# Kernel optimization log

Hardware: AMD Instinct MI355X
Metric: run time of the kernel (lower is better)

The kernel has to match this reference:

```python
import jax, jax.numpy as jnp
import numpy as np

N, E, F_IN, HID, HEADS, NT, B = 50000, 400000, 32, 64, 4, 20, 64
IN1 = F_IN + HID  # 96, conv1 input dim after concat with node-type embedding


def _glorot(key, shape):
    fan_in = shape[0]
    return jax.random.normal(key, shape, dtype=jnp.float32) / np.sqrt(fan_in)


def setup_inputs() -> dict:
    key = jax.random.key(0)
    ks = jax.random.split(key, 40)
    inp = {
        "x": jax.random.normal(ks[0], (N, F_IN), dtype=jnp.float32),
        "edge_index": jax.random.randint(ks[1], (2, E), 0, N, dtype=jnp.int32),
        "edge_attr": jax.random.normal(ks[2], (E,), dtype=jnp.float32),
        "batch": jnp.sort(jax.random.randint(ks[3], (N,), 0, B, dtype=jnp.int32)),
        "node_type": jax.random.randint(ks[4], (N,), 0, NT, dtype=jnp.int32),
        # parameters
        "node_emb": jax.random.normal(ks[5], (NT, HID), dtype=jnp.float32) * 0.1,
        "edge_W": _glorot(ks[6], (1, HID)), "edge_b": jnp.zeros((HID,), jnp.float32),
        # GATConv 1 (in=96, out=64, heads=4, edge_dim=64, concat=False)
        "W1": _glorot(ks[7], (IN1, HEADS * HID)),
        "att_src1": jax.random.normal(ks[8], (HEADS, HID), jnp.float32) * 0.1,
        "att_dst1": jax.random.normal(ks[9], (HEADS, HID), jnp.float32) * 0.1,
        "We1": _glorot(ks[10], (HID, HEADS * HID)),
        "att_e1": jax.random.normal(ks[11], (HEADS, HID), jnp.float32) * 0.1,
        "b1": jnp.zeros((HID,), jnp.float32),
        # GATConv 2 (in=64)
        "W2": _glorot(ks[12], (HID, HEADS * HID)),
        "att_src2": jax.random.normal(ks[13], (HEADS, HID), jnp.float32) * 0.1,
        "att_dst2": jax.random.normal(ks[14], (HEADS, HID), jnp.float32) * 0.1,
        "We2": _glorot(ks[15], (HID, HEADS * HID)),
        "att_e2": jax.random.normal(ks[16], (HEADS, HID), jnp.float32) * 0.1,
        "b2": jnp.zeros((HID,), jnp.float32),
        # SAGEConv (mean aggr): out = mean_agg @ Wl + x @ Wr + b
        "sage_Wl": _glorot(ks[17], (HID, HID)), "sage_Wr": _glorot(ks[18], (HID, HID)),
        "sage_b": jnp.zeros((HID,), jnp.float32),
        "lin1_W": _glorot(ks[19], (HID, HID)), "lin1_b": jnp.zeros((HID,), jnp.float32),
        "lin2_W": _glorot(ks[20], (HID, HID)), "lin2_b": jnp.zeros((HID,), jnp.float32),
        "tel_W": _glorot(ks[21], (HID, 1)), "tel_b": jnp.zeros((1,), jnp.float32),
        "comp_W": _glorot(ks[22], (HID, 1)), "comp_b": jnp.zeros((1,), jnp.float32),
        "pch_W": _glorot(ks[23], (HID, 1)), "pch_b": jnp.zeros((1,), jnp.float32),
    }
    return inp


def _gat(x, src, dst, edge_h, W, att_s, att_d, We, att_e, b):
    n = x.shape[0]
    h = (x @ W).reshape(n, HEADS, HID)                       # [N,H,C]
    a_s = (h * att_s).sum(-1)                                # [N,H]
    a_d = (h * att_d).sum(-1)
    e = (edge_h @ We).reshape(-1, HEADS, HID)                # [E,H,C]
    a_e = (e * att_e).sum(-1)                                # [E,H]
    alpha = jax.nn.leaky_relu(a_s[src] + a_d[dst] + a_e, 0.2)
    m = jax.ops.segment_max(alpha, dst, num_segments=n)
    m = jnp.where(jnp.isfinite(m), m, 0.0)
    ex = jnp.exp(alpha - m[dst])
    den = jax.ops.segment_sum(ex, dst, num_segments=n)
    alpha = ex / (den[dst] + 1e-16)                          # segment softmax per dst
    out = jax.ops.segment_sum(h[src] * alpha[..., None], dst, num_segments=n)
    return out.mean(axis=1) + b                              # concat=False -> head mean


def reference(x, edge_index, edge_attr, batch, node_type, node_emb, edge_W, edge_b,
              W1, att_src1, att_dst1, We1, att_e1, b1,
              W2, att_src2, att_dst2, We2, att_e2, b2,
              sage_Wl, sage_Wr, sage_b, lin1_W, lin1_b, lin2_W, lin2_b,
              tel_W, tel_b, comp_W, comp_b, pch_W, pch_b):
    src, dst = edge_index[0], edge_index[1]
    edge_h = edge_attr[:, None] @ edge_W + edge_b            # [E,HID]
    h = jnp.concatenate([x, node_emb[node_type]], axis=-1)   # [N,96]
    h = jax.nn.elu(_gat(h, src, dst, edge_h, W1, att_src1, att_dst1, We1, att_e1, b1))
    h = jax.nn.elu(_gat(h, src, dst, edge_h, W2, att_src2, att_dst2, We2, att_e2, b2))
    # SAGEConv with mean aggregation
    deg = jax.ops.segment_sum(jnp.ones((src.shape[0],), h.dtype), dst, num_segments=N)
    agg = jax.ops.segment_sum(h[src], dst, num_segments=N) / jnp.maximum(deg, 1.0)[:, None]
    h = jax.nn.elu(agg @ sage_Wl + h @ sage_Wr + sage_b)
    # global mean pool over graphs
    cnt = jax.ops.segment_sum(jnp.ones((N,), h.dtype), batch, num_segments=B)
    g = jax.ops.segment_sum(h, batch, num_segments=B) / jnp.maximum(cnt, 1.0)[:, None]
    g = jax.nn.elu(g @ lin1_W + lin1_b)                      # dropout is identity in eval
    g = g @ lin2_W + lin2_b
    return (g @ tel_W + tel_b, g @ comp_W + comp_b, g @ pch_W + pch_b)
```

## Files before the change

kernel.cpp:

```cpp
#include <hip/hip_runtime.h>
#include <hip/hip_bf16.h>


#define NN 50000
#define NE 400000
#define FIN 32
#define NBATCH 64

typedef __hip_bfloat16 bf16;
typedef short bf16x8 __attribute__((ext_vector_type(8)));
typedef float f32x4 __attribute__((ext_vector_type(4)));

__device__ __forceinline__ float b2f(bf16 v) { return __bfloat162float(v); }
__device__ __forceinline__ float lrelu(float x) { return x > 0.f ? x : 0.2f * x; }
__device__ __forceinline__ float eluf(float x) { return x > 0.f ? x : (expf(x) - 1.f); }

__device__ __forceinline__ float4 f4fma(float s, float4 w, float4 c) {
  c.x = fmaf(s, w.x, c.x); c.y = fmaf(s, w.y, c.y);
  c.z = fmaf(s, w.z, c.z); c.w = fmaf(s, w.w, c.w);
  return c;
}

__device__ __forceinline__ float4 upk4(uint2 u) {
  float4 f;
  f.x = __uint_as_float(u.x << 16);
  f.y = __uint_as_float(u.x & 0xffff0000u);
  f.z = __uint_as_float(u.y << 16);
  f.w = __uint_as_float(u.y & 0xffff0000u);
  return f;
}

__device__ __forceinline__ unsigned short bfbits(float f) {
  bf16 b = __float2bfloat16(f);
  unsigned short u;
  __builtin_memcpy(&u, &b, 2);
  return u;
}
__device__ __forceinline__ float hi_f(unsigned short u) {
  return __uint_as_float((unsigned int)u << 16);
}

__global__ __launch_bounds__(256) void k_pq(
    const float* __restrict__ We1, const float* __restrict__ atte1,
    const float* __restrict__ We2, const float* __restrict__ atte2,
    const float* __restrict__ edgeW, const float* __restrict__ edgeB,
    float* __restrict__ pq) {
  int t = threadIdx.x, h = t >> 6, c = t & 63;
  float sW1 = 0.f, sB1 = 0.f, sW2 = 0.f, sB2 = 0.f;
  for (int j = 0; j < 64; ++j) {
    float w = edgeW[j], b = edgeB[j];
    float we1 = We1[j * 256 + h * 64 + c];
    float we2 = We2[j * 256 + h * 64 + c];
    sW1 += w * we1; sB1 += b * we1;
    sW2 += w * we2; sB2 += b * we2;
  }
  float a1 = atte1[h * 64 + c], a2 = atte2[h * 64 + c];
  float p1 = sW1 * a1, q1 = sB1 * a1, p2 = sW2 * a2, q2 = sB2 * a2;
  for (int o = 32; o; o >>= 1) {
    p1 += __shfl_xor(p1, o); q1 += __shfl_xor(q1, o);
    p2 += __shfl_xor(p2, o); q2 += __shfl_xor(q2, o);
  }
  if (c == 0) { pq[h] = p1; pq[4 + h] = q1; pq[8 + h] = p2; pq[12 + h] = q2; }
}

__global__ void k_hist(const int* __restrict__ dst, int* __restrict__ cnt) {
  int e = blockIdx.x * 256 + threadIdx.x;
  if (e < NE) atomicAdd(&cnt[dst[e]], 1);
}

__global__ __launch_bounds__(1024) void k_scan(const int* __restrict__ cnt,
                                               int* __restrict__ off) {
  __shared__ int wsum[16];
  __shared__ int carry;
  int t = threadIdx.x, lane = t & 63, w = t >> 6;
  if (t == 0) { carry = 0; off[0] = 0; }
  __syncthreads();
  for (int base = 0; base < NN; base += 1024) {
    int idx = base + t;
    int v = (idx < NN) ? cnt[idx] : 0;
    int s = v;
    for (int o = 1; o < 64; o <<= 1) { int u = __shfl_up(s, o); if (lane >= o) s += u; }
    if (lane == 63) wsum[w] = s;
    __syncthreads();
    if (t < 16) {
      int ws = wsum[t];
      for (int o = 1; o < 16; o <<= 1) { int u = __shfl_up(ws, o); if (t >= o) ws += u; }
      wsum[t] = ws;
    }
    __syncthreads();
    int add = carry + (w ? wsum[w - 1] : 0);
    if (idx < NN) off[idx + 1] = add + s;
    __syncthreads();
    if (t == 0) carry += wsum[15];
    __syncthreads();
  }
}

__global__ void k_scatter(const int* __restrict__ src, const int* __restrict__ dst,
                          const float* __restrict__ ea, const int* __restrict__ off,
                          int* __restrict__ cur, int* __restrict__ csr_src,
                          float* __restrict__ csr_ea) {
  int e = blockIdx.x * 256 + threadIdx.x;
  if (e >= NE) return;
  int d = dst[e];
  int slot = off[d] + atomicAdd(&cur[d], 1);
  csr_src[slot] = src[e];
  csr_ea[slot] = ea[e];
}

__global__ __launch_bounds__(256) void k_splitA(
    const float* __restrict__ x, const int* __restrict__ ntype,
    const float* __restrict__ emb, unsigned short* __restrict__ Ah,
    unsigned short* __restrict__ Al) {
  const int total = NN * 96;
  for (int i = blockIdx.x * 256 + threadIdx.x; i < total; i += gridDim.x * 256) {
    int n = i / 96, k = i - n * 96;
    float v = (k < FIN) ? x[n * FIN + k] : emb[ntype[n] * 64 + (k - FIN)];
    unsigned short h = bfbits(v);
    Ah[i] = h;
    Al[i] = bfbits(v - hi_f(h));
  }
}

__global__ __launch_bounds__(256) void k_splitW(
    const float* __restrict__ W1, const float* __restrict__ W2,
    unsigned short* __restrict__ B1h, unsigned short* __restrict__ B1l,
    unsigned short* __restrict__ B2h, unsigned short* __restrict__ B2l) {
  int t = blockIdx.x * 256 + threadIdx.x;
  if (t < 256 * 96) {
    int n = t / 96, k = t - n * 96;
    float v = W1[k * 256 + n];
    unsigned short h = bfbits(v);
    B1h[t] = h; B1l[t] = bfbits(v - hi_f(h));
  }
  if (t < 256 * 64) {
    int n = t >> 6, k = t & 63;
    float v = W2[k * 256 + n];
    unsigned short h = bfbits(v);
    B2h[t] = h; B2l[t] = bfbits(v - hi_f(h));
  }
}

template <int K>
__global__ __launch_bounds__(256) void k_mm_mfma(
    const unsigned short* __restrict__ Ah, const unsigned short* __restrict__ Al,
    const unsigned short* __restrict__ Bh, const unsigned short* __restrict__ Bl,
    const float* __restrict__ atts, const float* __restrict__ attd,
    bf16* __restrict__ hmat, float* __restrict__ as_, float* __restrict__ ad_) {
  int m0 = blockIdx.x * 64;
  int w = threadIdx.x >> 6;
  int lane = threadIdx.x & 63;
  int lr = lane & 15;
  int lc = lane >> 4;
  float attsv[4], attdv[4];
  #pragma unroll
  for (int nt = 0; nt < 4; ++nt) {
    attsv[nt] = atts[w * 64 + nt * 16 + lr];
    attdv[nt] = attd[w * 64 + nt * 16 + lr];
  }
  f32x4 acc[4][4] = {};
  #pragma unroll
  for (int ks = 0; ks < K; ks += 32) {
    int koff = ks + lc * 8;
    bf16x8 ah[4], al[4], bh[4], bl[4];
    #pragma unroll
    for (int mt = 0; mt < 4; ++mt) {
      int m = m0 + mt * 16 + lr;
      if (m > NN - 1) m = NN - 1;
      ah[mt] = *reinterpret_cast<const bf16x8*>(&Ah[(size_t)m * K + koff]);
      al[mt] = *reinterpret_cast<const bf16x8*>(&Al[(size_t)m * K + koff]);
    }
    #pragma unroll
    for (int nt = 0; nt < 4; ++nt) {
      int n = w * 64 + nt * 16 + lr;
      bh[nt] = *reinterpret_cast<const bf16x8*>(&Bh[(size_t)n * K + koff]);
      bl[nt] = *reinterpret_cast<const bf16x8*>(&Bl[(size_t)n * K + koff]);
    }
    #pragma unroll
    for (int mt = 0; mt < 4; ++mt) {
      #pragma unroll
      for (int nt = 0; nt < 4; ++nt) {
        acc[mt][nt] = __builtin_amdgcn_mfma_f32_16x16x32_bf16(ah[mt], bh[nt], acc[mt][nt], 0, 0, 0);
        acc[mt][nt] = __builtin_amdgcn_mfma_f32_16x16x32_bf16(al[mt], bh[nt], acc[mt][nt], 0, 0, 0);
        acc[mt][nt] = __builtin_amdgcn_mfma_f32_16x16x32_bf16(ah[mt], bl[nt], acc[mt][nt], 0, 0, 0);
      }
    }
  }
  #pragma unroll
  for (int mt = 0; mt < 4; ++mt) {
    #pragma unroll
    for (int reg = 0; reg < 4; ++reg) {
      int row = m0 + mt * 16 + lc * 4 + reg;
      float sS = 0.f, sD = 0.f;
      #pragma unroll
      for (int nt = 0; nt < 4; ++nt) {
        float v = acc[mt][nt][reg];
        sS += v * attsv[nt];
        sD += v * attdv[nt];
      }
      for (int o = 1; o < 16; o <<= 1) {
        sS += __shfl_xor(sS, o);
        sD += __shfl_xor(sD, o);
      }
      if (row < NN) {
        #pragma unroll
        for (int nt = 0; nt < 4; ++nt)
          hmat[(size_t)row * 256 + w * 64 + nt * 16 + lr] =
              __float2bfloat16(acc[mt][nt][reg]);
        if (lr == 0) { as_[row * 4 + w] = sS; ad_[row * 4 + w] = sD; }
      }
    }
  }
}

__global__ __launch_bounds__(256) void k_gat(
    const int* __restrict__ off, const int* __restrict__ csr_src,
    const float* __restrict__ csr_ea, const float* __restrict__ as_,
    const float* __restrict__ ad_, const float* __restrict__ pq, int pqo,
    const bf16* __restrict__ hmat, const float* __restrict__ bias,
    float* __restrict__ outf, unsigned short* __restrict__ oph,
    unsigned short* __restrict__ opl) {
  __shared__ float wlds[4][256];
  int wv = threadIdx.x >> 6;
  int wid = (blockIdx.x << 2) + wv;
  int lane = threadIdx.x & 63;
  if (wid >= NN) return;
  int beg = off[wid], end = off[wid + 1];
  int deg = end - beg;
  int hsel = lane >> 4;
  float4 D = reinterpret_cast<const float4*>(ad_)[wid];
  float p0 = pq[pqo + 0], p1 = pq[pqo + 1], p2 = pq[pqo + 2], p3 = pq[pqo + 3];
  float q0 = pq[pqo + 4], q1 = pq[pqo + 5], q2 = pq[pqo + 6], q3 = pq[pqo + 7];
  float4 acc = {0.f, 0.f, 0.f, 0.f};

  if (deg <= 64) {
    bool valid = lane < deg;
    float lx = -INFINITY, ly = -INFINITY, lz = -INFINITY, lw = -INFINITY;
    if (valid) {
      int s = csr_src[beg + lane];
      float ea = csr_ea[beg + lane];
      float4 A = reinterpret_cast<const float4*>(as_)[s];
      lx = lrelu(A.x + D.x + ea * p0 + q0);
      ly = lrelu(A.y + D.y + ea * p1 + q1);
      lz = lrelu(A.z + D.z + ea * p2 + q2);
      lw = lrelu(A.w + D.w + ea * p3 + q3);
    }
    float m0 = lx, m1 = ly, m2 = lz, m3 = lw;
    for (int o = 32; o; o >>= 1) {
      m0 = fmaxf(m0, __shfl_xor(m0, o));
      m1 = fmaxf(m1, __shfl_xor(m1, o));
      m2 = fmaxf(m2, __shfl_xor(m2, o));
      m3 = fmaxf(m3, __shfl_xor(m3, o));
    }
    float w0 = valid ? __expf(lx - m0) : 0.f;
    float w1 = valid ? __expf(ly - m1) : 0.f;
    float w2 = valid ? __expf(lz - m2) : 0.f;
    float w3 = valid ? __expf(lw - m3) : 0.f;
    float s0 = w0, s1 = w1, s2 = w2, s3 = w3;
    for (int o = 32; o; o >>= 1) {
      s0 += __shfl_xor(s0, o); s1 += __shfl_xor(s1, o);
      s2 += __shfl_xor(s2, o); s3 += __shfl_xor(s3, o);
    }
    float4 wv4;
    wv4.x = w0 / (s0 + 1e-16f);
    wv4.y = w1 / (s1 + 1e-16f);
    wv4.z = w2 / (s2 + 1e-16f);
    wv4.w = w3 / (s3 + 1e-16f);
    reinterpret_cast<float4*>(&wlds[wv][0])[lane] = wv4;
    const float* wp = &wlds[wv][0];
    int j = 0;
    for (; j + 4 <= deg; j += 4) {
      int sA = csr_src[beg + j + 0];
      int sB = csr_src[beg + j + 1];
      int sC = csr_src[beg + j + 2];
      int sD = csr_src[beg + j + 3];
      float wA = wp[4 * (j + 0) + hsel];
      float wB = wp[4 * (j + 1) + hsel];
      float wC = wp[4 * (j + 2) + hsel];
      float wD = wp[4 * (j + 3) + hsel];
      uint2 uA = *reinterpret_cast<const uint2*>(&hmat[(size_t)sA * 256 + 4 * lane]);
      uint2 uB = *reinterpret_cast<const uint2*>(&hmat[(size_t)sB * 256 + 4 * lane]);
      uint2 uC = *reinterpret_cast<const uint2*>(&hmat[(size_t)sC * 256 + 4 * lane]);
      uint2 uD = *reinterpret_cast<const uint2*>(&hmat[(size_t)sD * 256 + 4 * lane]);
      acc = f4fma(wA, upk4(uA), acc);
      acc = f4fma(wB, upk4(uB), acc);
      acc = f4fma(wC, upk4(uC), acc);
      acc = f4fma(wD, upk4(uD), acc);
    }
    for (; j < deg; ++j) {
      int s = csr_src[beg + j];
      float w = wp[4 * j + hsel];
      uint2 u = *reinterpret_cast<const uint2*>(&hmat[(size_t)s * 256 + 4 * lane]);
      acc = f4fma(w, upk4(u), acc);
    }
  } else {
    float m0 = -INFINITY, m1 = -INFINITY, m2 = -INFINITY, m3 = -INFINITY;
    float s0 = 0.f, s1 = 0.f, s2 = 0.f, s3 = 0.f;
    for (int e = beg + lane; e < end; e += 64) {
      int s = csr_src[e];
      float ea = csr_ea[e];
      float4 A = reinterpret_cast<const float4*>(as_)[s];
      float lx = lrelu(A.x + D.x + ea * p0 + q0);
      float ly = lrelu(A.y + D.y + ea * p1 + q1);
      float lz = lrelu(A.z + D.z + ea * p2 + q2);
      float lw = lrelu(A.w + D.w + ea * p3 + q3);
      float nm;
      nm = fmaxf(m0, lx); s0 = s0 * __expf(m0 - nm) + __expf(lx - nm); m0 = nm;
      nm = fmaxf(m1, ly); s1 = s1 * __expf(m1 - nm) + __expf(ly - nm); m1 = nm;
      nm = fmaxf(m2, lz); s2 = s2 * __expf(m2 - nm) + __expf(lz - nm); m2 = nm;
      nm = fmaxf(m3, lw); s3 = s3 * __expf(m3 - nm) + __expf(lw - nm); m3 = nm;
    }
    for (int o = 32; o; o >>= 1) {
      float om, os, nm;
      om = __shfl_xor(m0, o); os = __shfl_xor(s0, o); nm = fmaxf(m0, om);
      s0 = s0 * __expf(fmaxf(m0 - nm, -80.f)) + os * __expf(fmaxf(om - nm, -80.f)); m0 = nm;
      om = __shfl_xor(m1, o); os = __shfl_xor(s1, o); nm = fmaxf(m1, om);
      s1 = s1 * __expf(fmaxf(m1 - nm, -80.f)) + os * __expf(fmaxf(om - nm, -80.f)); m1 = nm;
      om = __shfl_xor(m2, o); os = __shfl_xor(s2, o); nm = fmaxf(m2, om);
      s2 = s2 * __expf(fmaxf(m2 - nm, -80.f)) + os * __expf(fmaxf(om - nm, -80.f)); m2 = nm;
      om = __shfl_xor(m3, o); os = __shfl_xor(s3, o); nm = fmaxf(m3, om);
      s3 = s3 * __expf(fmaxf(m3 - nm, -80.f)) + os * __expf(fmaxf(om - nm, -80.f)); m3 = nm;
    }
    float i0 = 1.f / (s0 + 1e-16f), i1 = 1.f / (s1 + 1e-16f);
    float i2 = 1.f / (s2 + 1e-16f), i3 = 1.f / (s3 + 1e-16f);
    float Dh = hsel == 0 ? D.x : hsel == 1 ? D.y : hsel == 2 ? D.z : D.w;
    float ph = hsel == 0 ? p0 : hsel == 1 ? p1 : hsel == 2 ? p2 : p3;
    float qh = hsel == 0 ? q0 : hsel == 1 ? q1 : hsel == 2 ? q2 : q3;
    float mh = hsel == 0 ? m0 : hsel == 1 ? m1 : hsel == 2 ? m2 : m3;
    float ih = hsel == 0 ? i0 : hsel == 1 ? i1 : hsel == 2 ? i2 : i3;
    for (int j = beg; j < end; ++j) {
      int s = csr_src[j];
      float ea = csr_ea[j];
      float4 A = reinterpret_cast<const float4*>(as_)[s];
      float Ah = hsel == 0 ? A.x : hsel == 1 ? A.y : hsel == 2 ? A.z : A.w;
      float l = lrelu(Ah + Dh + ea * ph + qh);
      float w = __expf(l - mh) * ih;
      uint2 u = *reinterpret_cast<const uint2*>(&hmat[(size_t)s * 256 + 4 * lane]);
      acc = f4fma(w, upk4(u), acc);
    }
  }
  acc.x += __shfl_xor(acc.x, 16); acc.y += __shfl_xor(acc.y, 16);
  acc.z += __shfl_xor(acc.z, 16); acc.w += __shfl_xor(acc.w, 16);
  acc.x += __shfl_xor(acc.x, 32); acc.y += __shfl_xor(acc.y, 32);
  acc.z += __shfl_xor(acc.z, 32); acc.w += __shfl_xor(acc.w, 32);
  if (lane < 16) {
    float4 bv = reinterpret_cast<const float4*>(bias)[lane];
    float4 r;
    r.x = eluf(0.25f * acc.x + bv.x);
    r.y = eluf(0.25f * acc.y + bv.y);
    r.z = eluf(0.25f * acc.z + bv.z);
    r.w = eluf(0.25f * acc.w + bv.w);
    if (outf) reinterpret_cast<float4*>(&outf[(size_t)wid * 64])[lane] = r;
    if (oph) {
      ushort4 h4, l4;
      h4.x = bfbits(r.x); l4.x = bfbits(r.x - hi_f(h4.x));
      h4.y = bfbits(r.y); l4.y = bfbits(r.y - hi_f(h4.y));
      h4.z = bfbits(r.z); l4.z = bfbits(r.z - hi_f(h4.z));
      h4.w = bfbits(r.w); l4.w = bfbits(r.w - hi_f(h4.w));
      *reinterpret_cast<ushort4*>(&oph[(size_t)wid * 64 + lane * 4]) = h4;
      *reinterpret_cast<ushort4*>(&opl[(size_t)wid * 64 + lane * 4]) = l4;
    }
  }
}

__global__ __launch_bounds__(256) void k_agg(
    const int* __restrict__ off, const int* __restrict__ csr_src,
    const float* __restrict__ h3, float* __restrict__ agg) {
  int wid = (blockIdx.x << 2) + (threadIdx.x >> 6);
  int lane = threadIdx.x & 63;
  if (wid >= NN) return;
  int beg = off[wid], end = off[wid + 1];
  float acc = 0.f;
  int e = beg;
  for (; e + 4 <= end; e += 4) {
    int s0 = csr_src[e + 0], s1 = csr_src[e + 1];
    int s2 = csr_src[e + 2], s3 = csr_src[e + 3];
    float v0 = h3[(size_t)s0 * 64 + lane];
    float v1 = h3[(size_t)s1 * 64 + lane];
    float v2 = h3[(size_t)s2 * 64 + lane];
    float v3 = h3[(size_t)s3 * 64 + lane];
    acc += (v0 + v1) + (v2 + v3);
  }
  for (; e < end; ++e) acc += h3[(size_t)csr_src[e] * 64 + lane];
  agg[(size_t)wid * 64 + lane] = acc / fmaxf((float)(end - beg), 1.f);
}

__global__ __launch_bounds__(256) void k_sage_mm(
    const float* __restrict__ agg, const float* __restrict__ h3,
    const float* __restrict__ Wl, const float* __restrict__ Wr,
    const float* __restrict__ bias, float* __restrict__ out) {
  __shared__ float WlS[4096];
  __shared__ float WrS[4096];
  __shared__ float Ag[2048];
  __shared__ float Hr[2048];
  int t = threadIdx.x;
  for (int i = t; i < 4096; i += 256) { WlS[i] = Wl[i]; WrS[i] = Wr[i]; }
  int ct = t & 15, rg = t >> 4;
  float4 bv = reinterpret_cast<const float4*>(bias)[ct];
  for (int r0 = blockIdx.x * 32; r0 < NN; r0 += gridDim.x * 32) {
    for (int i = t; i < 2048; i += 256) {
      int n = r0 + (i >> 6);
      float va = 0.f, vh = 0.f;
      if (n < NN) {
        va = agg[(size_t)n * 64 + (i & 63)];
        vh = h3[(size_t)n * 64 + (i & 63)];
      }
      Ag[i] = va; Hr[i] = vh;
    }
    __syncthreads();
    float4 c0 = {0.f, 0.f, 0.f, 0.f}, c1 = c0;
    const float* a0 = &Ag[(rg * 2 + 0) * 64];
    const float* a1 = &Ag[(rg * 2 + 1) * 64];
    const float* h0 = &Hr[(rg * 2 + 0) * 64];
    const float* h1 = &Hr[(rg * 2 + 1) * 64];
    #pragma unroll 4
    for (int k = 0; k < 64; k += 4) {
      float4 wl0 = *reinterpret_cast<const float4*>(&WlS[(k + 0) * 64 + ct * 4]);
      float4 wl1 = *reinterpret_cast<const float4*>(&WlS[(k + 1) * 64 + ct * 4]);
      float4 wl2 = *reinterpret_cast<const float4*>(&WlS[(k + 2) * 64 + ct * 4]);
      float4 wl3 = *reinterpret_cast<const float4*>(&WlS[(k + 3) * 64 + ct * 4]);
      float4 wr0 = *reinterpret_cast<const float4*>(&WrS[(k + 0) * 64 + ct * 4]);
      float4 wr1 = *reinterpret_cast<const float4*>(&WrS[(k + 1) * 64 + ct * 4]);
      float4 wr2 = *reinterpret_cast<const float4*>(&WrS[(k + 2) * 64 + ct * 4]);
      float4 wr3 = *reinterpret_cast<const float4*>(&WrS[(k + 3) * 64 + ct * 4]);
      float4 aa0 = *reinterpret_cast<const float4*>(&a0[k]);
      float4 aa1 = *reinterpret_cast<const float4*>(&a1[k]);
      float4 hh0 = *reinterpret_cast<const float4*>(&h0[k]);
      float4 hh1 = *reinterpret_cast<const float4*>(&h1[k]);
      c0 = f4fma(aa0.x, wl0, c0); c0 = f4fma(aa0.y, wl1, c0);
      c0 = f4fma(aa0.z, wl2, c0); c0 = f4fma(aa0.w, wl3, c0);
      c0 = f4fma(hh0.x, wr0, c0); c0 = f4fma(hh0.y, wr1, c0);
      c0 = f4fma(hh0.z, wr2, c0); c0 = f4fma(hh0.w, wr3, c0);
      c1 = f4fma(aa1.x, wl0, c1); c1 = f4fma(aa1.y, wl1, c1);
      c1 = f4fma(aa1.z, wl2, c1); c1 = f4fma(aa1.w, wl3, c1);
      c1 = f4fma(hh1.x, wr0, c1); c1 = f4fma(hh1.y, wr1, c1);
      c1 = f4fma(hh1.z, wr2, c1); c1 = f4fma(hh1.w, wr3, c1);
    }
    int n0 = r0 + rg * 2;
    if (n0 + 0 < NN) {
      float4 r;
      r.x = eluf(c0.x + bv.x); r.y = eluf(c0.y + bv.y);
      r.z = eluf(c0.z + bv.z); r.w = eluf(c0.w + bv.w);
      *reinterpret_cast<float4*>(&out[(size_t)(n0 + 0) * 64 + ct * 4]) = r;
    }
    if (n0 + 1 < NN) {
      float4 r;
      r.x = eluf(c1.x + bv.x); r.y = eluf(c1.y + bv.y);
      r.z = eluf(c1.z + bv.z); r.w = eluf(c1.w + bv.w);
      *reinterpret_cast<float4*>(&out[(size_t)(n0 + 1) * 64 + ct * 4]) = r;
    }
    __syncthreads();
  }
}

__device__ __forceinline__ int lowerb(const int* __restrict__ a, int n, int key) {
  int lo = 0, hi = n;
  while (lo < hi) { int mid = (lo + hi) >> 1; if (a[mid] < key) lo = mid + 1; else hi = mid; }
  return lo;
}

__global__ __launch_bounds__(256) void k_pool(const float* __restrict__ hs,
                                              const int* __restrict__ batch,
                                              float* __restrict__ g) {
  int b = blockIdx.x;
  int lo = lowerb(batch, NN, b), hi = lowerb(batch, NN, b + 1);
  int t = threadIdx.x, lane = t & 63, w = t >> 6;
  float acc = 0.f;
  for (int n = lo + w; n < hi; n += 4) acc += hs[(size_t)n * 64 + lane];
  __shared__ float red[4][64];
  red[w][lane] = acc;
  __syncthreads();
  if (w == 0) {
    float v = red[0][lane] + red[1][lane] + red[2][lane] + red[3][lane];
    g[b * 64 + lane] = v / fmaxf((float)(hi - lo), 1.f);
  }
}

__global__ __launch_bounds__(256) void k_head(
    const float* __restrict__ g, const float* __restrict__ l1W,
    const float* __restrict__ l1b, const float* __restrict__ l2W,
    const float* __restrict__ l2b, const float* __restrict__ telW,
    const float* __restrict__ telb, const float* __restrict__ compW,
    const float* __restrict__ compb, const float* __restrict__ pchW,
    const float* __restrict__ pchb, float* __restrict__ out) {
  __shared__ float gS[4096];
  __shared__ float WS[4096];
  __shared__ float hS[4096];
  int t = threadIdx.x;
  for (int i = t; i < 4096; i += 256) { gS[i] = g[i]; WS[i] = l1W[i]; }
  __syncthreads();
  for (int i = t; i < 4096; i += 256) {
    int r = i >> 6, j = i & 63;
    float s = 0.f;
    for (int k = 0; k < 64; ++k) s += gS[r * 64 + k] * WS[k * 64 + j];
    hS[i] = eluf(s + l1b[j]);
  }
  __syncthreads();
  for (int i = t; i < 4096; i += 256) WS[i] = l2W[i];
  __syncthreads();
  for (int i = t; i < 4096; i += 256) {
    int r = i >> 6, j = i & 63;
    float s = 0.f;
    for (int k = 0; k < 64; ++k) s += hS[r * 64 + k] * WS[k * 64 + j];
    gS[i] = s + l2b[j];
  }
  __syncthreads();
  if (t < 192) {
    int head = t >> 6, r = t & 63;
    const float* Wv = head == 0 ? telW : (head == 1 ? compW : pchW);
    float bb = head == 0 ? telb[0] : (head == 1 ? compb[0] : pchb[0]);
    float s = 0.f;
    for (int k = 0; k < 64; ++k) s += gS[r * 64 + k] * Wv[k];
    out[t] = s + bb;
  }
}

extern "C" void kernel_launch(void* const* d_in, const int* in_sizes, int n_in,
                              void* d_out, int out_size, void* d_ws, size_t ws_size,
                              hipStream_t stream) {
  const float* x     = (const float*)d_in[0];
  const int*   eidx  = (const int*)d_in[1];
  const float* eattr = (const float*)d_in[2];
  const int*   batch = (const int*)d_in[3];
  const int*   ntype = (const int*)d_in[4];
  const float* nemb  = (const float*)d_in[5];
  const float* edgeW = (const float*)d_in[6];
  const float* edgeB = (const float*)d_in[7];
  const float* W1    = (const float*)d_in[8];
  const float* atts1 = (const float*)d_in[9];
  const float* attd1 = (const float*)d_in[10];
  const float* We1   = (const float*)d_in[11];
  const float* atte1 = (const float*)d_in[12];
  const float* b1    = (const float*)d_in[13];
  const float* W2    = (const float*)d_in[14];
  const float* atts2 = (const float*)d_in[15];
  const float* attd2 = (const float*)d_in[16];
  const float* We2   = (const float*)d_in[17];
  const float* atte2 = (const float*)d_in[18];
  const float* b2    = (const float*)d_in[19];
  const float* sageWl = (const float*)d_in[20];
  const float* sageWr = (const float*)d_in[21];
  const float* sageB  = (const float*)d_in[22];
  const float* l1W = (const float*)d_in[23];
  const float* l1b = (const float*)d_in[24];
  const float* l2W = (const float*)d_in[25];
  const float* l2b = (const float*)d_in[26];
  const float* telW  = (const float*)d_in[27];
  const float* telb  = (const float*)d_in[28];
  const float* compW = (const float*)d_in[29];
  const float* compb = (const float*)d_in[30];
  const float* pchW  = (const float*)d_in[31];
  const float* pchb  = (const float*)d_in[32];

  char* wp = (char*)d_ws;
  auto alloc = [&](size_t bytes) -> char* {
    char* p = wp;
    wp += (bytes + 255) & ~(size_t)255;
    return p;
  };
  float*  pq      = (float*)alloc(16 * 4);
  int*    cnt     = (int*)alloc((size_t)NN * 4);
  int*    off     = (int*)alloc(((size_t)NN + 1) * 4);
  int*    csr_src = (int*)alloc((size_t)NE * 4);
  float*  csr_ea  = (float*)alloc((size_t)NE * 4);
  float*  as_     = (float*)alloc((size_t)NN * 16);
  float*  ad_     = (float*)alloc((size_t)NN * 16);
  bf16*   hmat    = (bf16*)alloc((size_t)NN * 256 * 2);
  float*  nodeB   = (float*)alloc((size_t)NN * 64 * 4);
  float*  aggbuf  = (float*)alloc((size_t)NN * 64 * 4);
  unsigned short* B1h = (unsigned short*)alloc(256 * 96 * 2);
  unsigned short* B1l = (unsigned short*)alloc(256 * 96 * 2);
  unsigned short* B2h = (unsigned short*)alloc(256 * 64 * 2);
  unsigned short* B2l = (unsigned short*)alloc(256 * 64 * 2);
  char* R = alloc((size_t)NN * 96 * 2 * 2);
  unsigned short* A1h = (unsigned short*)R;
  unsigned short* A1l = A1h + (size_t)NN * 96;
  unsigned short* A2h = (unsigned short*)R;
  unsigned short* A2l = A2h + (size_t)NN * 64;
  float* sageout = (float*)R;
  float* gbuf = (float*)alloc(64 * 64 * 4);

  const int* srcI = eidx;
  const int* dstI = eidx + NE;

  hipMemsetAsync(cnt, 0, (size_t)NN * 4, stream);
  k_pq<<<1, 256, 0, stream>>>(We1, atte1, We2, atte2, edgeW, edgeB, pq);
  k_hist<<<(NE + 255) / 256, 256, 0, stream>>>(dstI, cnt);
  k_scan<<<1, 1024, 0, stream>>>(cnt, off);
  hipMemsetAsync(cnt, 0, (size_t)NN * 4, stream);
  k_scatter<<<(NE + 255) / 256, 256, 0, stream>>>(srcI, dstI, eattr, off, cnt,
                                                  csr_src, csr_ea);
  k_splitW<<<96, 256, 0, stream>>>(W1, W2, B1h, B1l, B2h, B2l);
  k_splitA<<<2048, 256, 0, stream>>>(x, ntype, nemb, A1h, A1l);
  k_mm_mfma<96><<<(NN + 63) / 64, 256, 0, stream>>>(
      A1h, A1l, B1h, B1l, atts1, attd1, hmat, as_, ad_);
  k_gat<<<NN / 4, 256, 0, stream>>>(off, csr_src, csr_ea, as_, ad_, pq, 0,
                                    hmat, b1, nullptr, A2h, A2l);
  k_mm_mfma<64><<<(NN + 63) / 64, 256, 0, stream>>>(
      A2h, A2l, B2h, B2l, atts2, attd2, hmat, as_, ad_);
  k_gat<<<NN / 4, 256, 0, stream>>>(off, csr_src, csr_ea, as_, ad_, pq, 8,
                                    hmat, b2, nodeB, nullptr, nullptr);
  k_agg<<<NN / 4, 256, 0, stream>>>(off, csr_src, nodeB, aggbuf);
  k_sage_mm<<<1024, 256, 0, stream>>>(aggbuf, nodeB, sageWl, sageWr, sageB,
                                      sageout);
  k_pool<<<NBATCH, 256, 0, stream>>>(sageout, batch, gbuf);
  k_head<<<1, 256, 0, stream>>>(gbuf, l1W, l1b, l2W, l2b, telW, telb, compW,
                                compb, pchW, pchb, (float*)d_out);
}
```

Measured before the change: 490.3 us.

## Parallelize global mean pool with chunked atomic accumulation across many blocks

Replaces the 64-block pooling kernel, where each block binary-searched and summed one graph's nodes, with a kernel that gives each wavefront a 32-node chunk. Each wavefront accumulates a run-length partial sum per batch id and adds it to the output with atomics. The division by node count moves into the head kernel, which computes counts by binary search. The output buffer is zeroed with an extra memset, and atomic float adds make the summation order nondeterministic.

```diff
diff --git a/kernel.cpp b/kernel.cpp
--- a/kernel.cpp
+++ b/kernel.cpp
@@ -453,41 +453,54 @@
   }
 }
 
+__global__ __launch_bounds__(256) void k_pool2(const float* __restrict__ hs,
+                                               const int* __restrict__ batch,
+                                               float* __restrict__ g) {
+  int cid = (blockIdx.x << 2) + (threadIdx.x >> 6);
+  int lane = threadIdx.x & 63;
+  int n0 = cid * 32;
+  if (n0 >= NN) return;
+  int n1 = n0 + 32 < NN ? n0 + 32 : NN;
+  int cur = batch[n0];
+  float acc = 0.f;
+  for (int n = n0; n < n1; ++n) {
+    int b = batch[n];
+    if (b != cur) {
+      atomicAdd(&g[cur * 64 + lane], acc);
+      acc = 0.f;
+      cur = b;
+    }
+    acc += hs[(size_t)n * 64 + lane];
+  }
+  atomicAdd(&g[cur * 64 + lane], acc);
+}
+
 __device__ __forceinline__ int lowerb(const int* __restrict__ a, int n, int key) {
   int lo = 0, hi = n;
   while (lo < hi) { int mid = (lo + hi) >> 1; if (a[mid] < key) lo = mid + 1; else hi = mid; }
   return lo;
 }
 
-__global__ __launch_bounds__(256) void k_pool(const float* __restrict__ hs,
-                                              const int* __restrict__ batch,
-                                              float* __restrict__ g) {
-  int b = blockIdx.x;
-  int lo = lowerb(batch, NN, b), hi = lowerb(batch, NN, b + 1);
-  int t = threadIdx.x, lane = t & 63, w = t >> 6;
-  float acc = 0.f;
-  for (int n = lo + w; n < hi; n += 4) acc += hs[(size_t)n * 64 + lane];
-  __shared__ float red[4][64];
-  red[w][lane] = acc;
-  __syncthreads();
-  if (w == 0) {
-    float v = red[0][lane] + red[1][lane] + red[2][lane] + red[3][lane];
-    g[b * 64 + lane] = v / fmaxf((float)(hi - lo), 1.f);
-  }
-}
-
 __global__ __launch_bounds__(256) void k_head(
-    const float* __restrict__ g, const float* __restrict__ l1W,
-    const float* __restrict__ l1b, const float* __restrict__ l2W,
-    const float* __restrict__ l2b, const float* __restrict__ telW,
-    const float* __restrict__ telb, const float* __restrict__ compW,
-    const float* __restrict__ compb, const float* __restrict__ pchW,
-    const float* __restrict__ pchb, float* __restrict__ out) {
+    const float* __restrict__ g, const int* __restrict__ batch,
+    const float* __restrict__ l1W, const float* __restrict__ l1b,
+    const float* __restrict__ l2W, const float* __restrict__ l2b,
+    const float* __restrict__ telW, const float* __restrict__ telb,
+    const float* __restrict__ compW, const float* __restrict__ compb,
+    const float* __restrict__ pchW, const float* __restrict__ pchb,
+    float* __restrict__ out) {
   __shared__ float gS[4096];
   __shared__ float WS[4096];
   __shared__ float hS[4096];
+  __shared__ float invc[64];
   int t = threadIdx.x;
-  for (int i = t; i < 4096; i += 256) { gS[i] = g[i]; WS[i] = l1W[i]; }
+  if (t < 64) {
+    int lo = lowerb(batch, NN, t), hi = lowerb(batch, NN, t + 1);
+    invc[t] = 1.f / fmaxf((float)(hi - lo), 1.f);
+  }
+  for (int i = t; i < 4096; i += 256) WS[i] = l1W[i];
+  __syncthreads();
+  for (int i = t; i < 4096; i += 256) gS[i] = g[i] * invc[i >> 6];
   __syncthreads();
   for (int i = t; i < 4096; i += 256) {
     int r = i >> 6, j = i & 63;
@@ -584,6 +597,7 @@
   const int* dstI = eidx + NE;
 
   hipMemsetAsync(cnt, 0, (size_t)NN * 4, stream);
+  hipMemsetAsync(gbuf, 0, 64 * 64 * 4, stream);
   k_pq<<<1, 256, 0, stream>>>(We1, atte1, We2, atte2, edgeW, edgeB, pq);
   k_hist<<<(NE + 255) / 256, 256, 0, stream>>>(dstI, cnt);
   k_scan<<<1, 1024, 0, stream>>>(cnt, off);
@@ -603,7 +617,7 @@
   k_agg<<<NN / 4, 256, 0, stream>>>(off, csr_src, nodeB, aggbuf);
   k_sage_mm<<<1024, 256, 0, stream>>>(aggbuf, nodeB, sageWl, sageWr, sageB,
                                       sageout);
-  k_pool<<<NBATCH, 256, 0, stream>>>(sageout, batch, gbuf);
-  k_head<<<1, 256, 0, stream>>>(gbuf, l1W, l1b, l2W, l2b, telW, telb, compW,
-                                compb, pchW, pchb, (float*)d_out);
-}
+  k_pool2<<<((NN + 31) / 32 + 3) / 4, 256, 0, stream>>>(sageout, batch, gbuf);
+  k_head<<<1, 256, 0, stream>>>(gbuf, batch, l1W, l1b, l2W, l2b, telW, telb,
+                                compW, compb, pchW, pchb, (float*)d_out);
+}
```

New measurement: 468.2 us. 1.05x faster.
